# Kernel tuning notes

Hardware: AMD Instinct MI355X
Metric: run time of the kernel (lower is better)

The kernel has to match this reference:

```python
import jax, jax.numpy as jnp
import numpy as np

B, N, D, H = 8, 1024, 1024, 16
DH = D // H
REL_VOCAB = 6  # stadia + 2
NEG_INF = -1e9


def setup_inputs() -> dict:
    key = jax.random.key(0)
    ks = jax.random.split(key, 8)
    hid = jax.random.normal(ks[0], (B, N, D), dtype=jnp.float32)
    adj = jax.random.randint(ks[1], (B, N, N), 0, 2, dtype=jnp.int32)
    relative_pos = jax.random.randint(ks[2], (B, N, N), 0, REL_VOCAB, dtype=jnp.int32)
    s = 1.0 / np.sqrt(D)
    Wq = jax.random.normal(ks[3], (D, D), dtype=jnp.float32) * s
    Wk = jax.random.normal(ks[4], (D, D), dtype=jnp.float32) * s
    Wv = jax.random.normal(ks[5], (D, D), dtype=jnp.float32) * s
    rel_table = jax.random.normal(ks[6], (REL_VOCAB, 1), dtype=jnp.float32)
    ln_gamma = jnp.ones((D,), dtype=jnp.float32)
    ln_beta = jnp.zeros((D,), dtype=jnp.float32)
    return {"hid": hid, "adj": adj, "relative_pos": relative_pos,
            "Wq": Wq, "Wk": Wk, "Wv": Wv, "rel_table": rel_table,
            "ln_gamma": ln_gamma, "ln_beta": ln_beta}


def _layer_norm(x, gamma, beta, eps=1e-5):
    mu = jnp.mean(x, axis=-1, keepdims=True)
    var = jnp.var(x, axis=-1, keepdims=True)
    return (x - mu) * jax.lax.rsqrt(var + eps) * gamma + beta


def reference(hid, adj, relative_pos, Wq, Wk, Wv, rel_table, ln_gamma, ln_beta):
    # relative position bias: embedding dim 1, squeezed -> [B, N, N]
    rel_bias = rel_table[relative_pos][..., 0]
    # projections, split into heads: [B, N, H, DH]
    q = (hid @ Wq).reshape(B, N, H, DH)
    k = (hid @ Wk).reshape(B, N, H, DH)
    v = (hid @ Wv).reshape(B, N, H, DH)
    # scores [B, H, N, N], scaled by sqrt(key_dim) = sqrt(D)
    scores = jnp.einsum('bqhd,bkhd->bhqk', q, k) / jnp.sqrt(jnp.float32(D))
    scores = scores + rel_bias[:, None, :, :]
    mask = (adj != 0)[:, None, :, :]
    scores = jnp.where(mask, scores, NEG_INF)
    attn = jax.nn.softmax(scores, axis=-1)
    out = jnp.einsum('bhqk,bkhd->bqhd', attn, v).reshape(B, N, D)
    out = jax.nn.relu(out) + hid  # activation + residual
    return _layer_norm(out, ln_gamma, ln_beta)
```

## Files before the change

### kernel.cpp

```cpp
#include <hip/hip_runtime.h>
#include <math.h>

#define Bc 8
#define Nc 1024
#define Dc 1024
#define Hc 16
#define DHc 64
#define NEGINF -1e9f

typedef unsigned int  u32;
typedef unsigned short u16;
typedef unsigned long long u64;
typedef u16  u16x8 __attribute__((ext_vector_type(8)));
typedef u16  u16x4 __attribute__((ext_vector_type(4)));
typedef u32  u32x2 __attribute__((ext_vector_type(2)));
typedef __bf16 bf16x8 __attribute__((ext_vector_type(8)));
typedef float f32x4 __attribute__((ext_vector_type(4)));

__device__ __forceinline__ u16 f2bf(float f) {
    u32 u = __builtin_bit_cast(u32, f);
    u += 0x7fffu + ((u >> 16) & 1u);
    return (u16)(u >> 16);
}
__device__ __forceinline__ float bf2f(u16 b) {
    return __builtin_bit_cast(float, (u32)b << 16);
}
__device__ __forceinline__ u32 pack2bf(float lo, float hi) {
    return __builtin_amdgcn_perm(__builtin_bit_cast(u32, hi),
                                 __builtin_bit_cast(u32, lo), 0x07060302u);
}

__device__ __forceinline__ void glds16(const u16* g, const u16* l) {
    __builtin_amdgcn_global_load_lds(
        (const __attribute__((address_space(1))) void*)(u64)g,
        (__attribute__((address_space(3))) void*)(u32)(u64)l, 16, 0, 0);
}

__global__ __launch_bounds__(256) void prep_fused(
    const int* __restrict__ adj, const int* __restrict__ relpos,
    const float* __restrict__ rel_table, u16* __restrict__ bias,
    const float* __restrict__ hid, u16* __restrict__ hidb,
    const float* __restrict__ Wq, const float* __restrict__ Wk,
    const float* __restrict__ Wv, u16* __restrict__ WqT,
    u16* __restrict__ WkT, u16* __restrict__ WvT)
{
    const int blk = blockIdx.x;
    const int t = threadIdx.x;

    if (blk < 8192) {
        __shared__ float tbl[8];
        if (t < 6) tbl[t] = rel_table[t];
        __syncthreads();
        int i = blk * 256 + t;
        int pos4 = i << 2;
        int row  = pos4 >> 10;
        int p    = pos4 & 1023;
        int blkb = p & ~63;
        int m    = (p & 63) >> 2;
        size_t base = ((size_t)row << 10) + blkb + m;
        u16x4 o;
#pragma unroll
        for (int j = 0; j < 4; ++j) {
            int a  = adj[base + 16 * j];
            int rp = relpos[base + 16 * j];
            o[j] = a ? f2bf(tbl[rp]) : f2bf(NEGINF);
        }
        ((u16x4*)bias)[i] = o;
    } else if (blk < 12288) {
        int idx = (blk - 8192) * 256 + t;
        float4 a = ((const float4*)hid)[2 * idx];
        float4 b = ((const float4*)hid)[2 * idx + 1];
        u16x8 o;
        o[0] = f2bf(a.x); o[1] = f2bf(a.y); o[2] = f2bf(a.z); o[3] = f2bf(a.w);
        o[4] = f2bf(b.x); o[5] = f2bf(b.y); o[6] = f2bf(b.z); o[7] = f2bf(b.w);
        ((u16x8*)hidb)[idx] = o;
    } else {
        __shared__ float tile[32][33];
        const int wb = blk - 12288;
        const int x = wb & 31, y = (wb >> 5) & 31, z = wb >> 10;
        const float* W; u16* WT;
        if (z == 0)      { W = Wq; WT = WqT; }
        else if (z == 1) { W = Wk; WT = WkT; }
        else             { W = Wv; WT = WvT; }
        const int tx = t & 31, ty = t >> 5;
        const int n0 = x * 32, k0 = y * 32;
#pragma unroll
        for (int i = 0; i < 4; ++i) {
            int r = ty + i * 8;
            tile[r][tx] = W[(size_t)(k0 + r) * Dc + n0 + tx];
        }
        __syncthreads();
#pragma unroll
        for (int i = 0; i < 4; ++i) {
            int n = ty + i * 8;
            WT[(size_t)(n0 + n) * Dc + k0 + tx] = f2bf(tile[tx][n]);
        }
    }
}

__global__ __launch_bounds__(256) void qkv_mfma(
    const u16* __restrict__ hidb, const u16* __restrict__ WqT,
    const u16* __restrict__ WkT, const u16* __restrict__ WvT,
    u16* __restrict__ qo, u16* __restrict__ ko, u16* __restrict__ vo)
{
    __shared__ u16 As[128 * 64];
    __shared__ u16 Bs[128 * 64];

    const int bx = blockIdx.x, by = blockIdx.y;
    const int z = bx >> 3;
    const int c0 = (bx << 7) & 1023;
    const int row0 = by << 7;
    const u16* WT; u16* out;
    if (z == 0)      { WT = WqT; out = qo; }
    else if (z == 1) { WT = WkT; out = ko; }
    else             { WT = WvT; out = vo; }

    const int tid = threadIdx.x;
    const int wave = tid >> 6, lane = tid & 63;
    const int g = lane >> 4, li = lane & 15;
    const int wr = wave >> 1, wc = wave & 1;
    const int lr = lane >> 3, ls = lane & 7;
    const int sseg = ls ^ lr;

    const u16* pa = hidb + (size_t)(row0 + wave * 32 + lr) * Dc + sseg * 8;
    const u16* pb = WT   + (size_t)(c0   + wave * 32 + lr) * Dc + sseg * 8;
    u16* la = &As[(wave * 32) * 64];
    u16* lb = &Bs[(wave * 32) * 64];

    f32x4 acc[4][4] = {};

    const int swz = (li & 7);

    for (int kt = 0; kt < Dc; kt += 64) {
        __syncthreads();
#pragma unroll
        for (int i = 0; i < 4; ++i) {
            glds16(pa + kt + i * 8 * Dc, la + i * 8 * 64);
            glds16(pb + kt + i * 8 * Dc, lb + i * 8 * 64);
        }
        __syncthreads();
#pragma unroll
        for (int ks = 0; ks < 2; ++ks) {
            const int soff = ((ks * 4 + g) ^ swz) * 8;
            bf16x8 af[4], bf[4];
#pragma unroll
            for (int mi = 0; mi < 4; ++mi)
                af[mi] = *(const bf16x8*)&As[(wr * 64 + mi * 16 + li) * 64 + soff];
#pragma unroll
            for (int nj = 0; nj < 4; ++nj)
                bf[nj] = *(const bf16x8*)&Bs[(wc * 64 + nj * 16 + li) * 64 + soff];
#pragma unroll
            for (int mi = 0; mi < 4; ++mi)
#pragma unroll
                for (int nj = 0; nj < 4; ++nj)
                    acc[mi][nj] = __builtin_amdgcn_mfma_f32_16x16x32_bf16(
                        af[mi], bf[nj], acc[mi][nj], 0, 0, 0);
        }
    }

    const int b = row0 >> 10;

    if (z != 2) {
        const int h2 = (c0 + wc * 64) >> 6;
        const int nbase = (row0 & 1023) + wr * 64 + g * 4;
#pragma unroll
        for (int mi = 0; mi < 4; ++mi)
#pragma unroll
            for (int rr = 0; rr < 4; ++rr) {
                int n = nbase + mi * 16 + rr;
                u32x2 pk;
                pk.x = (u32)f2bf(acc[mi][0][rr]) | ((u32)f2bf(acc[mi][1][rr]) << 16);
                pk.y = (u32)f2bf(acc[mi][2][rr]) | ((u32)f2bf(acc[mi][3][rr]) << 16);
                *(u32x2*)(out + ((size_t)(b * Hc + h2) * Nc + n) * DHc + 4 * li) = pk;
            }
    } else {
        __syncthreads();
        u16* T = ((wave & 2) ? Bs : As) + (wave & 1) * 4096;
#pragma unroll
        for (int mi = 0; mi < 4; ++mi)
#pragma unroll
            for (int rr = 0; rr < 4; ++rr) {
                int r = mi * 16 + g * 4 + rr;
                int pp = ((r & 15) << 2) | (r >> 4);
#pragma unroll
                for (int nj = 0; nj < 4; ++nj) {
                    int c = nj * 16 + li;
                    T[c * 64 + ((((pp >> 3) ^ (c & 7)) << 3) | (pp & 7))]
                        = f2bf(acc[mi][nj][rr]);
                }
            }
        const int nseg = ls ^ lr;
#pragma unroll
        for (int i = 0; i < 8; ++i) {
            int cl = i * 8 + lr;
            u16x8 val = *(const u16x8*)&T[cl * 64 + ls * 8];
            int cz = c0 + wc * 64 + cl;
            int n = (row0 & 1023) + wr * 64 + nseg * 8;
            *(u16x8*)&out[(((size_t)(b * Hc + (cz >> 6)) * DHc + (cz & 63)) * Nc) + n] = val;
        }
    }
}

__global__ __launch_bounds__(256, 3) void attn_mfma(
    const u16* __restrict__ q, const u16* __restrict__ k,
    const u16* __restrict__ v, const u16* __restrict__ bias,
    float* __restrict__ attn_out)
{
    __shared__ u16 Ks[2][64 * 64];
    __shared__ u16 VTs[2][64 * 64];
    __shared__ u16 PQ[128 * 72];

    const int tid = threadIdx.x;
    const int w = tid >> 6, lane = tid & 63;
    const int g = lane >> 4, li = lane & 15;
    const int lr8 = lane >> 3, ls8 = lane & 7;
    const int lseg = ls8 ^ lr8;

    const int id = blockIdx.x;
    const int b  = id & 7;
    const int r_ = id >> 3;
    const int h  = r_ & 15;
    const int qt = r_ >> 4;
    const int q0 = qt << 7;

    const float scale = 0.03125f;
    const u16* kbase = k + (size_t)(b * Hc + h) * Nc * DHc;
    const u16* vbase = v + (size_t)(b * Hc + h) * DHc * Nc;
    const u16* brow  = bias + ((size_t)(b * Nc) + q0 + w * 32) * Nc + 4 * li;

    {
        const u16* kp = kbase + (size_t)(w * 16 + lr8) * DHc + lseg * 8;
        const u16* vp = vbase + (size_t)(w * 16 + lr8) * Nc + lseg * 8;
        glds16(kp,           &Ks[0][(w * 16) * 64]);
        glds16(kp + 8 * DHc, &Ks[0][(w * 16) * 64 + 8 * 64]);
        glds16(vp,           &VTs[0][(w * 16) * 64]);
        glds16(vp + 8 * Nc,  &VTs[0][(w * 16) * 64 + 8 * 64]);
    }

    {
        const int sr = tid >> 1;
        const int sh = (tid & 1) * 32;
        const u16* qp = q + ((size_t)((b * Hc + h) * Nc) + q0 + sr) * DHc + sh;
        u16x8 a0 = *(const u16x8*)qp;
        u16x8 a1 = *(const u16x8*)(qp + 8);
        u16x8 a2 = *(const u16x8*)(qp + 16);
        u16x8 a3 = *(const u16x8*)(qp + 24);
        u16* dst = &PQ[sr * 72 + sh];
        *(u16x8*)(dst)      = a0; *(u16x8*)(dst + 8)  = a1;
        *(u16x8*)(dst + 16) = a2; *(u16x8*)(dst + 24) = a3;
    }

    u16x4 brv[2][4];
#pragma unroll
    for (int mt = 0; mt < 2; ++mt)
#pragma unroll
        for (int r = 0; r < 4; ++r)
            brv[mt][r] = *(const u16x4*)&brow[(size_t)(mt * 16 + g * 4 + r) * Nc];

    bf16x8 qf[2][2];
#pragma unroll
    for (int mt = 0; mt < 2; ++mt)
#pragma unroll
        for (int ks = 0; ks < 2; ++ks)
            qf[mt][ks] = *(const bf16x8*)&PQ[(w * 32 + mt * 16 + li) * 72 + ks * 32 + g * 8];

    f32x4 o_[2][4] = {};
    float lsum[2][4] = {};

    for (int it = 0; it < 16; ++it) {
        const int cur = it & 1;
        __syncthreads();

        u16x4 brn[2][4];
        if (it < 15) {
            const int k1 = (it + 1) * 64;
            const u16* kp = kbase + (size_t)(k1 + w * 16 + lr8) * DHc + lseg * 8;
            const u16* vp = vbase + (size_t)(w * 16 + lr8) * Nc + k1 + lseg * 8;
            u16* kl = &Ks[cur ^ 1][(w * 16) * 64];
            u16* vl = &VTs[cur ^ 1][(w * 16) * 64];
            glds16(kp,           kl);
            glds16(kp + 8 * DHc, kl + 8 * 64);
            glds16(vp,           vl);
            glds16(vp + 8 * Nc,  vl + 8 * 64);
#pragma unroll
            for (int mt = 0; mt < 2; ++mt)
#pragma unroll
                for (int r = 0; r < 4; ++r)
                    brn[mt][r] = *(const u16x4*)&brow[(size_t)(mt * 16 + g * 4 + r) * Nc + k1];
        }

        f32x4 sacc[2][4] = {};
#pragma unroll
        for (int ks = 0; ks < 2; ++ks) {
            const int so = (((ks << 2) | g) ^ (li & 7)) << 3;
#pragma unroll
            for (int nt = 0; nt < 4; ++nt) {
                bf16x8 kf = *(const bf16x8*)&Ks[cur][(nt * 16 + li) * 64 + so];
                sacc[0][nt] = __builtin_amdgcn_mfma_f32_16x16x32_bf16(qf[0][ks], kf, sacc[0][nt], 0, 0, 0);
                sacc[1][nt] = __builtin_amdgcn_mfma_f32_16x16x32_bf16(qf[1][ks], kf, sacc[1][nt], 0, 0, 0);
            }
        }

#pragma unroll
        for (int mt = 0; mt < 2; ++mt)
#pragma unroll
            for (int r = 0; r < 4; ++r) {
                const int qrl = mt * 16 + g * 4 + r;
                float pv[4];
#pragma unroll
                for (int nt = 0; nt < 4; ++nt) {
                    float sv = sacc[mt][nt][r] * scale + bf2f(brv[mt][r][nt]);
                    pv[nt] = __expf(sv);
                    lsum[mt][r] += pv[nt];
                }
                u32* dst = (u32*)&PQ[(w * 32 + qrl) * 72 + li * 4];
                dst[0] = pack2bf(pv[0], pv[1]);
                dst[1] = pack2bf(pv[2], pv[3]);
            }

#pragma unroll
        for (int ks = 0; ks < 2; ++ks) {
            const int so = (((ks << 2) | g) ^ (li & 7)) << 3;
            bf16x8 pa0 = *(const bf16x8*)&PQ[(w * 32 + li) * 72 + ks * 32 + g * 8];
            bf16x8 pa1 = *(const bf16x8*)&PQ[(w * 32 + 16 + li) * 72 + ks * 32 + g * 8];
#pragma unroll
            for (int j = 0; j < 4; ++j) {
                bf16x8 vf = *(const bf16x8*)&VTs[cur][(j * 16 + li) * 64 + so];
                o_[0][j] = __builtin_amdgcn_mfma_f32_16x16x32_bf16(pa0, vf, o_[0][j], 0, 0, 0);
                o_[1][j] = __builtin_amdgcn_mfma_f32_16x16x32_bf16(pa1, vf, o_[1][j], 0, 0, 0);
            }
        }

        if (it < 15) {
#pragma unroll
            for (int mt = 0; mt < 2; ++mt)
#pragma unroll
                for (int r = 0; r < 4; ++r)
                    brv[mt][r] = brn[mt][r];
        }
    }

#pragma unroll
    for (int mt = 0; mt < 2; ++mt)
#pragma unroll
        for (int r = 0; r < 4; ++r) {
            float l = lsum[mt][r];
            l += __shfl_xor(l, 1);
            l += __shfl_xor(l, 2);
            l += __shfl_xor(l, 4);
            l += __shfl_xor(l, 8);
            float inv = 1.f / l;
            int qrow = q0 + w * 32 + mt * 16 + g * 4 + r;
            float* op = attn_out + ((size_t)b * Nc + qrow) * Dc + h * DHc;
#pragma unroll
            for (int j = 0; j < 4; ++j)
                op[j * 16 + li] = o_[mt][j][r] * inv;
        }
}

__global__ __launch_bounds__(256) void ln_kernel(
    const float* attn_out, const float* __restrict__ hid,
    const float* __restrict__ gamma, const float* __restrict__ beta,
    float* out)
{
    const int row = blockIdx.x;
    const int t = threadIdx.x;

    float4 av = *(const float4*)&attn_out[(size_t)row * Dc + t * 4];
    float4 hv = *(const float4*)&hid[(size_t)row * Dc + t * 4];
    float x0 = fmaxf(av.x, 0.f) + hv.x;
    float x1 = fmaxf(av.y, 0.f) + hv.y;
    float x2 = fmaxf(av.z, 0.f) + hv.z;
    float x3 = fmaxf(av.w, 0.f) + hv.w;

    float s1 = x0 + x1 + x2 + x3;
    float s2 = x0 * x0 + x1 * x1 + x2 * x2 + x3 * x3;
#pragma unroll
    for (int off = 1; off < 64; off <<= 1) {
        s1 += __shfl_xor(s1, off);
        s2 += __shfl_xor(s2, off);
    }
    __shared__ float w1[4], w2[4];
    int lane = t & 63, wid = t >> 6;
    if (lane == 0) { w1[wid] = s1; w2[wid] = s2; }
    __syncthreads();
    s1 = w1[0] + w1[1] + w1[2] + w1[3];
    s2 = w2[0] + w2[1] + w2[2] + w2[3];

    float mu  = s1 * (1.f / 1024.f);
    float var = s2 * (1.f / 1024.f) - mu * mu;
    float rstd = rsqrtf(var + 1e-5f);

    float4 g  = *(const float4*)&gamma[t * 4];
    float4 be = *(const float4*)&beta[t * 4];
    float4 r4;
    r4.x = (x0 - mu) * rstd * g.x + be.x;
    r4.y = (x1 - mu) * rstd * g.y + be.y;
    r4.z = (x2 - mu) * rstd * g.z + be.z;
    r4.w = (x3 - mu) * rstd * g.w + be.w;
    *(float4*)&out[(size_t)row * Dc + t * 4] = r4;
}

extern "C" void kernel_launch(void* const* d_in, const int* in_sizes, int n_in,
                              void* d_out, int out_size, void* d_ws, size_t ws_size,
                              hipStream_t stream) {
    const float* hid       = (const float*)d_in[0];
    const int*   adj       = (const int*)d_in[1];
    const int*   relpos    = (const int*)d_in[2];
    const float* Wq        = (const float*)d_in[3];
    const float* Wk        = (const float*)d_in[4];
    const float* Wv        = (const float*)d_in[5];
    const float* rel_table = (const float*)d_in[6];
    const float* gamma     = (const float*)d_in[7];
    const float* beta      = (const float*)d_in[8];
    float* out = (float*)d_out;

    const size_t per  = (size_t)Bc * Hc * Nc * DHc;
    const size_t wsz  = (size_t)Dc * Dc;
    u16* qb   = (u16*)d_ws;
    u16* kb   = qb + per;
    u16* vb   = kb + per;
    u16* bias = vb + per;
    u16* hidb = bias + (size_t)Bc * Nc * Nc;
    u16* wqT  = hidb + (size_t)Bc * Nc * Dc;
    u16* wkT  = wqT + wsz;
    u16* wvT  = wkT + wsz;

    prep_fused<<<15360, 256, 0, stream>>>(adj, relpos, rel_table, bias,
                                          hid, hidb, Wq, Wk, Wv, wqT, wkT, wvT);
    qkv_mfma<<<dim3(24, 64), 256, 0, stream>>>(hidb, wqT, wkT, wvT, qb, kb, vb);
    attn_mfma<<<1024, 256, 0, stream>>>(qb, kb, vb, bias, out);
    ln_kernel<<<Bc * Nc, 256, 0, stream>>>(out, hid, gamma, beta, out);
}
```

Measured before the change: 284.9 us.

## Fold softmax scale into Q, use raw exp2, shrink attention LDS for occupancy

Folds the 1/sqrt(D) scale into the Q projection epilogue and the log2(e) factor into the bias table, so the softmax uses a raw v_exp_f32 with one fma. The attention kernel drops V double-buffering and the padded P/Q buffer in favour of an XOR-swizzled layout, cutting LDS so launch bounds can rise from 3 to 4 blocks per CU. K prefetch and bias loads move to the end of each iteration, and s_setprio is placed around the MFMA phases. The QKV grid is also reordered so consecutive blocks walk rows rather than columns. Loading V within the iteration and adding an extra barrier may expose memory latency that the old double buffer hid.

Result: slower. 295.1 us (+3.6%).

```diff
diff --git a/kernel.cpp b/kernel.cpp
--- a/kernel.cpp
+++ b/kernel.cpp
@@ -7,6 +7,7 @@
 #define Hc 16
 #define DHc 64
 #define NEGINF -1e9f
+#define LOG2E 1.44269504f
 
 typedef unsigned int  u32;
 typedef unsigned short u16;
@@ -28,6 +29,11 @@
 __device__ __forceinline__ u32 pack2bf(float lo, float hi) {
     return __builtin_amdgcn_perm(__builtin_bit_cast(u32, hi),
                                  __builtin_bit_cast(u32, lo), 0x07060302u);
+}
+__device__ __forceinline__ float exp2_raw(float x) {
+    float r;
+    asm("v_exp_f32 %0, %1" : "=v"(r) : "v"(x));
+    return r;
 }
 
 __device__ __forceinline__ void glds16(const u16* g, const u16* l) {
@@ -49,7 +55,7 @@
 
     if (blk < 8192) {
         __shared__ float tbl[8];
-        if (t < 6) tbl[t] = rel_table[t];
+        if (t < 6) tbl[t] = rel_table[t] * LOG2E;
         __syncthreads();
         int i = blk * 256 + t;
         int pos4 = i << 2;
@@ -106,14 +112,15 @@
     __shared__ u16 As[128 * 64];
     __shared__ u16 Bs[128 * 64];
 
-    const int bx = blockIdx.x, by = blockIdx.y;
-    const int z = bx >> 3;
-    const int c0 = (bx << 7) & 1023;
-    const int row0 = by << 7;
+    const int by = blockIdx.y;
+    const int z = by >> 3;
+    const int c0 = (by & 7) << 7;
+    const int row0 = blockIdx.x << 7;
     const u16* WT; u16* out;
     if (z == 0)      { WT = WqT; out = qo; }
     else if (z == 1) { WT = WkT; out = ko; }
     else             { WT = WvT; out = vo; }
+    const float qsc = (z == 0) ? 0.03125f : 1.0f;
 
     const int tid = threadIdx.x;
     const int wave = tid >> 6, lane = tid & 63;
@@ -169,8 +176,8 @@
             for (int rr = 0; rr < 4; ++rr) {
                 int n = nbase + mi * 16 + rr;
                 u32x2 pk;
-                pk.x = (u32)f2bf(acc[mi][0][rr]) | ((u32)f2bf(acc[mi][1][rr]) << 16);
-                pk.y = (u32)f2bf(acc[mi][2][rr]) | ((u32)f2bf(acc[mi][3][rr]) << 16);
+                pk.x = (u32)f2bf(acc[mi][0][rr] * qsc) | ((u32)f2bf(acc[mi][1][rr] * qsc) << 16);
+                pk.y = (u32)f2bf(acc[mi][2][rr] * qsc) | ((u32)f2bf(acc[mi][3][rr] * qsc) << 16);
                 *(u32x2*)(out + ((size_t)(b * Hc + h2) * Nc + n) * DHc + 4 * li) = pk;
             }
     } else {
@@ -196,19 +203,19 @@
             u16x8 val = *(const u16x8*)&T[cl * 64 + ls * 8];
             int cz = c0 + wc * 64 + cl;
             int n = (row0 & 1023) + wr * 64 + nseg * 8;
-            *(u16x8*)&out[(((size_t)(b * Hc + (cz >> 6)) * DHc + (cz & 63)) * Nc) + n] = val;
-        }
-    }
-}
-
-__global__ __launch_bounds__(256, 3) void attn_mfma(
+            *(u16x8*)&vo[(((size_t)(b * Hc + (cz >> 6)) * DHc + (cz & 63)) * Nc) + n] = val;
+        }
+    }
+}
+
+__global__ __launch_bounds__(256, 4) void attn_mfma(
     const u16* __restrict__ q, const u16* __restrict__ k,
     const u16* __restrict__ v, const u16* __restrict__ bias,
     float* __restrict__ attn_out)
 {
     __shared__ u16 Ks[2][64 * 64];
-    __shared__ u16 VTs[2][64 * 64];
-    __shared__ u16 PQ[128 * 72];
+    __shared__ u16 VTs[64 * 64];
+    __shared__ u16 PQ[128 * 64];
 
     const int tid = threadIdx.x;
     const int w = tid >> 6, lane = tid & 63;
@@ -223,31 +230,26 @@
     const int qt = r_ >> 4;
     const int q0 = qt << 7;
 
-    const float scale = 0.03125f;
     const u16* kbase = k + (size_t)(b * Hc + h) * Nc * DHc;
     const u16* vbase = v + (size_t)(b * Hc + h) * DHc * Nc;
     const u16* brow  = bias + ((size_t)(b * Nc) + q0 + w * 32) * Nc + 4 * li;
 
     {
         const u16* kp = kbase + (size_t)(w * 16 + lr8) * DHc + lseg * 8;
-        const u16* vp = vbase + (size_t)(w * 16 + lr8) * Nc + lseg * 8;
         glds16(kp,           &Ks[0][(w * 16) * 64]);
         glds16(kp + 8 * DHc, &Ks[0][(w * 16) * 64 + 8 * 64]);
-        glds16(vp,           &VTs[0][(w * 16) * 64]);
-        glds16(vp + 8 * Nc,  &VTs[0][(w * 16) * 64 + 8 * 64]);
     }
 
     {
         const int sr = tid >> 1;
         const int sh = (tid & 1) * 32;
+        const int sw = (sr & 7) << 3;
         const u16* qp = q + ((size_t)((b * Hc + h) * Nc) + q0 + sr) * DHc + sh;
-        u16x8 a0 = *(const u16x8*)qp;
-        u16x8 a1 = *(const u16x8*)(qp + 8);
-        u16x8 a2 = *(const u16x8*)(qp + 16);
-        u16x8 a3 = *(const u16x8*)(qp + 24);
-        u16* dst = &PQ[sr * 72 + sh];
-        *(u16x8*)(dst)      = a0; *(u16x8*)(dst + 8)  = a1;
-        *(u16x8*)(dst + 16) = a2; *(u16x8*)(dst + 24) = a3;
+        u16* dst = &PQ[sr * 64];
+        *(u16x8*)(dst + ((sh +  0) ^ sw)) = *(const u16x8*)(qp);
+        *(u16x8*)(dst + ((sh +  8) ^ sw)) = *(const u16x8*)(qp + 8);
+        *(u16x8*)(dst + ((sh + 16) ^ sw)) = *(const u16x8*)(qp + 16);
+        *(u16x8*)(dst + ((sh + 24) ^ sw)) = *(const u16x8*)(qp + 24);
     }
 
     u16x4 brv[2][4];
@@ -262,7 +264,8 @@
     for (int mt = 0; mt < 2; ++mt)
 #pragma unroll
         for (int ks = 0; ks < 2; ++ks)
-            qf[mt][ks] = *(const bf16x8*)&PQ[(w * 32 + mt * 16 + li) * 72 + ks * 32 + g * 8];
+            qf[mt][ks] = *(const bf16x8*)&PQ[(w * 32 + mt * 16 + li) * 64
+                                            + ((ks * 32 + g * 8) ^ ((li & 7) << 3))];
 
     f32x4 o_[2][4] = {};
     float lsum[2][4] = {};
@@ -271,25 +274,14 @@
         const int cur = it & 1;
         __syncthreads();
 
-        u16x4 brn[2][4];
-        if (it < 15) {
-            const int k1 = (it + 1) * 64;
-            const u16* kp = kbase + (size_t)(k1 + w * 16 + lr8) * DHc + lseg * 8;
-            const u16* vp = vbase + (size_t)(w * 16 + lr8) * Nc + k1 + lseg * 8;
-            u16* kl = &Ks[cur ^ 1][(w * 16) * 64];
-            u16* vl = &VTs[cur ^ 1][(w * 16) * 64];
-            glds16(kp,           kl);
-            glds16(kp + 8 * DHc, kl + 8 * 64);
-            glds16(vp,           vl);
-            glds16(vp + 8 * Nc,  vl + 8 * 64);
-#pragma unroll
-            for (int mt = 0; mt < 2; ++mt)
-#pragma unroll
-                for (int r = 0; r < 4; ++r)
-                    brn[mt][r] = *(const u16x4*)&brow[(size_t)(mt * 16 + g * 4 + r) * Nc + k1];
+        {
+            const u16* vp = vbase + (size_t)(w * 16 + lr8) * Nc + it * 64 + lseg * 8;
+            glds16(vp,          &VTs[(w * 16) * 64]);
+            glds16(vp + 8 * Nc, &VTs[(w * 16) * 64 + 8 * 64]);
         }
 
         f32x4 sacc[2][4] = {};
+        __builtin_amdgcn_s_setprio(1);
 #pragma unroll
         for (int ks = 0; ks < 2; ++ks) {
             const int so = (((ks << 2) | g) ^ (li & 7)) << 3;
@@ -300,43 +292,54 @@
                 sacc[1][nt] = __builtin_amdgcn_mfma_f32_16x16x32_bf16(qf[1][ks], kf, sacc[1][nt], 0, 0, 0);
             }
         }
+        __builtin_amdgcn_s_setprio(0);
 
 #pragma unroll
         for (int mt = 0; mt < 2; ++mt)
 #pragma unroll
             for (int r = 0; r < 4; ++r) {
-                const int qrl = mt * 16 + g * 4 + r;
+                const int qrl = w * 32 + mt * 16 + g * 4 + r;
                 float pv[4];
 #pragma unroll
                 for (int nt = 0; nt < 4; ++nt) {
-                    float sv = sacc[mt][nt][r] * scale + bf2f(brv[mt][r][nt]);
-                    pv[nt] = __expf(sv);
+                    pv[nt] = exp2_raw(fmaf(sacc[mt][nt][r], LOG2E,
+                                           bf2f(brv[mt][r][nt])));
                     lsum[mt][r] += pv[nt];
                 }
-                u32* dst = (u32*)&PQ[(w * 32 + qrl) * 72 + li * 4];
+                u32* dst = (u32*)&PQ[(qrl & ~7) * 64
+                                     + (((qrl & 7) * 64 + li * 4) ^ ((qrl & 7) << 3))];
                 dst[0] = pack2bf(pv[0], pv[1]);
                 dst[1] = pack2bf(pv[2], pv[3]);
             }
 
+        __syncthreads();
+
+        __builtin_amdgcn_s_setprio(1);
 #pragma unroll
         for (int ks = 0; ks < 2; ++ks) {
             const int so = (((ks << 2) | g) ^ (li & 7)) << 3;
-            bf16x8 pa0 = *(const bf16x8*)&PQ[(w * 32 + li) * 72 + ks * 32 + g * 8];
-            bf16x8 pa1 = *(const bf16x8*)&PQ[(w * 32 + 16 + li) * 72 + ks * 32 + g * 8];
+            const int po = (ks * 32 + g * 8) ^ ((li & 7) << 3);
+            bf16x8 pa0 = *(const bf16x8*)&PQ[(w * 32 + li) * 64 + po];
+            bf16x8 pa1 = *(const bf16x8*)&PQ[(w * 32 + 16 + li) * 64 + po];
 #pragma unroll
             for (int j = 0; j < 4; ++j) {
-                bf16x8 vf = *(const bf16x8*)&VTs[cur][(j * 16 + li) * 64 + so];
+                bf16x8 vf = *(const bf16x8*)&VTs[(j * 16 + li) * 64 + so];
                 o_[0][j] = __builtin_amdgcn_mfma_f32_16x16x32_bf16(pa0, vf, o_[0][j], 0, 0, 0);
                 o_[1][j] = __builtin_amdgcn_mfma_f32_16x16x32_bf16(pa1, vf, o_[1][j], 0, 0, 0);
             }
         }
+        __builtin_amdgcn_s_setprio(0);
 
         if (it < 15) {
+            const int k1 = (it + 1) * 64;
+            const u16* kp = kbase + (size_t)(k1 + w * 16 + lr8) * DHc + lseg * 8;
+            glds16(kp,           &Ks[cur ^ 1][(w * 16) * 64]);
+            glds16(kp + 8 * DHc, &Ks[cur ^ 1][(w * 16) * 64 + 8 * 64]);
 #pragma unroll
             for (int mt = 0; mt < 2; ++mt)
 #pragma unroll
                 for (int r = 0; r < 4; ++r)
-                    brv[mt][r] = brn[mt][r];
+                    brv[mt][r] = *(const u16x4*)&brow[(size_t)(mt * 16 + g * 4 + r) * Nc + k1];
         }
     }
 
@@ -428,7 +431,7 @@
 
     prep_fused<<<15360, 256, 0, stream>>>(adj, relpos, rel_table, bias,
                                           hid, hidb, Wq, Wk, Wv, wqT, wkT, wvT);
-    qkv_mfma<<<dim3(24, 64), 256, 0, stream>>>(hidb, wqT, wkT, wvT, qb, kb, vb);
+    qkv_mfma<<<dim3(64, 24), 256, 0, stream>>>(hidb, wqT, wkT, wvT, qb, kb, vb);
     attn_mfma<<<1024, 256, 0, stream>>>(qb, kb, vb, bias, out);
     ln_kernel<<<Bc * Nc, 256, 0, stream>>>(out, hid, gamma, beta, out);
 }
```
